# Kernel tuning notes

Hardware: AMD Instinct MI355X
Metric: run time of the kernel (lower is better)

## Reference

```python
import jax, jax.numpy as jnp
import numpy as np

HID = 128          # hidden_channels
NG = 256           # number of graphs in batch
NL = 50000         # ligand nodes
NP = 150000        # protein nodes
E = 500000         # edges (ligand->protein); rev edges are the reverse
RBF_COUNT = 8
D_MAX = 5.0


def _rbf(d):
    # d: [E] distances -> [E, 8] gaussian RBF expansion (D_min=0, D_max=5, count=8)
    mu = jnp.linspace(0.0, D_MAX, RBF_COUNT)
    sigma = D_MAX / RBF_COUNT
    return jnp.exp(-(((d[:, None] - mu[None, :]) / sigma) ** 2))


def setup_inputs() -> dict:
    key = jax.random.key(0)
    ks = jax.random.split(key, 24)
    s = 0.05
    inp = {
        "x_ligand": jax.random.normal(ks[0], (NL, 44), jnp.float32),
        "x_protein": jax.random.normal(ks[1], (NP, 44), jnp.float32),
        "edge_attr": jax.random.uniform(ks[2], (E, 1), jnp.float32) * D_MAX,
        "edge_src": jax.random.randint(ks[3], (E,), 0, NL),
        "edge_dst": jax.random.randint(ks[4], (E,), 0, NP),
        "ligand_batch": jnp.sort(jax.random.randint(ks[5], (NL,), 0, NG)),
        # shared node embedding and edge embedding
        "W_node": jax.random.normal(ks[6], (44, HID), jnp.float32) * s,
        "W_el": jax.random.normal(ks[7], (1, 8), jnp.float32) * s,
        # 6 NConvs: index = layer*2 + (0: ligand->protein, 1: protein->ligand)
        "Wb": jax.random.normal(ks[8], (6, RBF_COUNT, HID), jnp.float32) * s,
        "bb": jnp.zeros((6, HID), jnp.float32),
        "Wn": jax.random.normal(ks[9], (6, HID, HID), jnp.float32) * s,
        "Ws": jax.random.normal(ks[10], (6, HID, HID), jnp.float32) * s,
        "bconv": jnp.zeros((6, HID), jnp.float32),
        # edge MLP: [2*HID+8 -> 512 -> 128] (BN in eval mode = identity, dropout off)
        "W1": jax.random.normal(ks[11], (2 * HID + 8, 512), jnp.float32) * s,
        "b1": jnp.zeros((512,), jnp.float32),
        "W2": jax.random.normal(ks[12], (512, 128), jnp.float32) * s,
        "b2": jnp.zeros((128,), jnp.float32),
        # lin_mpl: 128 -> out_channels//2 = 128
        "Wm": jax.random.normal(ks[13], (128, 128), jnp.float32) * s,
        "bm": jnp.zeros((128,), jnp.float32),
    }
    return inp


def _nconv(x_src, x_dst, src, dst, n_dst, rbf_feat, Wb_i, bb_i, Wn_i, Ws_i, b_i):
    # base = SiLU(Linear(rbf)); message = fc_neigh(base * x_j); aggr = mean over dst
    base = jax.nn.silu(rbf_feat @ Wb_i + bb_i)              # [E, HID]
    msg = (base * x_src[src]) @ Wn_i                         # gather + mul + GEMM
    agg = jax.ops.segment_sum(msg, dst, num_segments=n_dst)  # [n_dst, HID]
    deg = jax.ops.segment_sum(jnp.ones((src.shape[0], 1), msg.dtype), dst,
                              num_segments=n_dst)
    agg = agg / jnp.maximum(deg, 1.0)
    return x_dst @ Ws_i + agg + b_i


def reference(x_ligand, x_protein, edge_attr, edge_src, edge_dst, ligand_batch,
              W_node, W_el, Wb, bb, Wn, Ws, bconv, W1, b1, W2, b2, Wm, bm):
    lrelu = lambda v: jax.nn.leaky_relu(v, 0.01)
    xl = x_ligand @ W_node   # [NL, HID]
    xp = x_protein @ W_node  # [NP, HID]
    rbf_feat = _rbf(jnp.squeeze(edge_attr, -1))  # [E, 8]

    xl_sum = jnp.zeros_like(xl)
    xp_sum = jnp.zeros_like(xp)
    for l in range(3):
        i_lp, i_pl = 2 * l, 2 * l + 1
        # HeteroConv applies both edge types to the SAME input dict
        xp_new = lrelu(_nconv(xl, xp, edge_src, edge_dst, NP, rbf_feat,
                              Wb[i_lp], bb[i_lp], Wn[i_lp], Ws[i_lp], bconv[i_lp]))
        xl_new = lrelu(_nconv(xp, xl, edge_dst, edge_src, NL, rbf_feat,
                              Wb[i_pl], bb[i_pl], Wn[i_pl], Ws[i_pl], bconv[i_pl]))
        xl, xp = xl_new, xp_new
        xl_sum = xl_sum + xl
        xp_sum = xp_sum + xp

    # edge readout on the ligand->protein edges
    edge_repr = jnp.concatenate([xl_sum[edge_src], xp_sum[edge_dst]], axis=-1)
    d_pl = edge_attr @ W_el                                   # [E, 8]
    edge_repr = jnp.concatenate([edge_repr, d_pl], axis=1)    # [E, 2*HID+8]
    # edge_mlp (eval mode: BatchNorm identity, dropout off)
    m_pl = jax.nn.relu(edge_repr @ W1 + b1) @ W2 + b2         # [E, 128]
    w_pl = jnp.tanh(m_pl @ Wm + bm)                           # [E, 128]
    edge_batch = ligand_batch[edge_src]
    m_w = jax.ops.segment_sum(w_pl * m_pl, edge_batch, num_segments=NG)
    m_max = jax.ops.segment_max(m_pl, edge_batch, num_segments=NG)
    m_max = jnp.where(jnp.isfinite(m_max), m_max, 0.0)        # empty segments -> 0
    return jnp.concatenate([m_w, m_max], axis=1)              # [NG, 256]
```

## Files before the change

### kernel.cpp

```cpp
#include <hip/hip_runtime.h>
#include <hip/hip_bf16.h>


#define NLn 50000
#define NPn 150000
#define En  500000
#define NBL 1563
#define NBP 4688

typedef __attribute__((ext_vector_type(8))) short short8;
typedef __attribute__((ext_vector_type(4))) float float4v;

__device__ __forceinline__ float bf2f(unsigned short u){ return __uint_as_float(((unsigned)u) << 16); }
__device__ __forceinline__ float bflo(unsigned u){ return __uint_as_float(u << 16); }
__device__ __forceinline__ float bfhi(unsigned u){ return __uint_as_float(u & 0xffff0000u); }
__device__ __forceinline__ unsigned short f2bf(float f){
  __hip_bfloat16 h = __float2bfloat16(f);
  return *reinterpret_cast<unsigned short*>(&h);
}
__device__ __forceinline__ unsigned encf(float f){
  unsigned u = __float_as_uint(f);
  return (u & 0x80000000u) ? ~u : (u | 0x80000000u);
}
__device__ __forceinline__ float tanh_fast(float x){
  return 1.f - 2.f/(__expf(2.f*x) + 1.f);
}

__global__ __launch_bounds__(256) void k_embed(
    const float* __restrict__ Xl, const float* __restrict__ Xp,
    const float* __restrict__ Wnode,
    unsigned short* __restrict__ xl0, unsigned short* __restrict__ xp0){
  __shared__ float xs[1408];
  int b = blockIdx.x, tid = threadIdx.x;
  bool isL = b < NBL;
  const float* X = isL ? Xl : Xp;
  unsigned short* out = isL ? xl0 : xp0;
  int n = isL ? NLn : NPn;
  int n0 = (isL ? b : b - NBL) * 32;
  int nrows = n - n0; if (nrows > 32) nrows = 32;
  int nflt = nrows * 44;
  const float4* Xv = (const float4*)(X + (size_t)n0*44);
  for (int j = tid; j*4 < nflt; j += 256){
    float4 v = Xv[j];
    xs[j*4+0]=v.x; xs[j*4+1]=v.y; xs[j*4+2]=v.z; xs[j*4+3]=v.w;
  }
  __syncthreads();
  int c = tid & 127, half = tid >> 7;
  float acc[16];
  #pragma unroll
  for (int r=0;r<16;r++) acc[r]=0.f;
  const float* xrow = xs + half*16*44;
  #pragma unroll 4
  for (int k=0;k<44;k++){
    float w = Wnode[k*128 + c];
    #pragma unroll
    for (int r=0;r<16;r++) acc[r] += xrow[r*44 + k] * w;
  }
  int rbase = n0 + half*16;
  #pragma unroll
  for (int r=0;r<16;r++){
    int nn = rbase + r;
    if (nn < n) out[(size_t)nn*128 + c] = f2bf(acc[r]);
  }
}

__global__ __launch_bounds__(256) void k_prep(
    unsigned* __restrict__ cntz, unsigned* __restrict__ mmaxz, unsigned* __restrict__ outz,
    const float* __restrict__ Wel, const float* __restrict__ W1, float* __restrict__ vvec,
    const float* __restrict__ W2, unsigned short* __restrict__ w2t,
    const float* __restrict__ Wm, unsigned short* __restrict__ wmt,
    const float* __restrict__ Ws, const float* __restrict__ Wn,
    unsigned short* __restrict__ wcat, unsigned short* __restrict__ w1t,
    const float* __restrict__ Wb, const float* __restrict__ bb,
    unsigned short* __restrict__ lut){
  int b = blockIdx.x, tid = threadIdx.x;
  if (b < 196){
    for (long i = (long)b*256 + tid; i < 200000; i += 196*256) cntz[i] = 0u;
  } else if (b < 324){
    mmaxz[(b-196)*256 + tid] = 0u;
  } else if (b < 580){
    outz[(b-324)*256 + tid] = 0u;
  } else if (b < 582){
    int j = (b-580)*256 + tid;
    float s = 0.f;
    #pragma unroll
    for (int r=0;r<8;r++) s += Wel[r]*W1[(256+r)*512 + j];
    vvec[j] = s;
  } else if (b < 838){
    int gid = (b-582)*256 + tid;
    int n = gid >> 9, k = gid & 511;
    w2t[n*512 + k] = f2bf(W2[k*128 + n]);
  } else if (b < 902){
    int gid = (b-838)*256 + tid;
    int n = gid >> 7, k = gid & 127;
    wmt[n*128 + k] = f2bf(Wm[k*128 + n]);
  } else if (b < 1670){
    int gid = (b-902)*256 + tid;
    int i = gid >> 15, rem = gid & 32767;
    int n = rem >> 8, k = rem & 255;
    float v = (k < 128) ? Ws[i*16384 + k*128 + n] : Wn[i*16384 + (k-128)*128 + n];
    wcat[gid] = f2bf(v);
  } else if (b < 2182){
    int gid = (b-1670)*256 + tid;
    int part = gid >> 16, rem = gid & 65535;
    int n = rem >> 7, k = rem & 127;
    w1t[gid] = f2bf(W1[(part*128 + k)*512 + n]);
  } else {
    int gid = (b-2182)*256 + tid;
    int c = gid & 127, bin = (gid >> 7) & 4095, i = gid >> 19;
    float d = ((float)bin + 0.5f) * 0.001220703125f;
    float s = bb[i*128 + c];
    #pragma unroll
    for (int j=0;j<8;j++){
      float a = (d - 0.7142857143f*(float)j) * 1.6f;
      s += __expf(-a*a) * Wb[i*1024 + j*128 + c];
    }
    lut[gid] = f2bf(s / (1.f + __expf(-s)));
  }
}

__global__ __launch_bounds__(256) void k_count(const int* __restrict__ esrc,
    const int* __restrict__ edst, unsigned* __restrict__ cntL, unsigned* __restrict__ cntP){
  int e = blockIdx.x*256 + threadIdx.x;
  if (e >= En) return;
  atomicAdd(&cntL[esrc[e]], 1u);
  atomicAdd(&cntP[edst[e]], 1u);
}
__global__ __launch_bounds__(256) void k_cs2(const unsigned* __restrict__ cntL,
    unsigned* __restrict__ rowptrL, unsigned* __restrict__ bsumL,
    const unsigned* __restrict__ cntP, unsigned* __restrict__ rowptrP,
    unsigned* __restrict__ bsumP){
  bool isL = blockIdx.x < 49;
  const unsigned* cnt = isL ? cntL : cntP;
  unsigned* rowptr = isL ? rowptrL : rowptrP;
  unsigned* bsum = isL ? bsumL : bsumP;
  int n = isL ? NLn : NPn;
  int lb = isL ? blockIdx.x : blockIdx.x - 49;
  __shared__ unsigned ts[256];
  int tid = threadIdx.x;
  int base = lb*1024 + tid*4;
  unsigned v[4], run = 0;
  #pragma unroll
  for (int j=0;j<4;j++){ v[j] = run; run += (base+j < n) ? cnt[base+j] : 0u; }
  ts[tid] = run; __syncthreads();
  for (int off=1; off<256; off<<=1){
    unsigned t = (tid>=off) ? ts[tid-off] : 0u; __syncthreads();
    ts[tid] += t; __syncthreads();
  }
  unsigned excl = ts[tid] - run;
  #pragma unroll
  for (int j=0;j<4;j++) if (base+j < n) rowptr[base+j] = excl + v[j];
  if (tid == 255) bsum[lb] = ts[255];
}
__global__ void k_sb2(unsigned* __restrict__ bsumL, unsigned* __restrict__ bsumP){
  unsigned* bsum = blockIdx.x ? bsumP : bsumL;
  int nc = blockIdx.x ? 147 : 49;
  __shared__ unsigned ts[256];
  int tid = threadIdx.x;
  unsigned x = (tid < nc) ? bsum[tid] : 0u;
  ts[tid] = x; __syncthreads();
  for (int off=1; off<256; off<<=1){
    unsigned t = (tid>=off) ? ts[tid-off] : 0u; __syncthreads();
    ts[tid] += t; __syncthreads();
  }
  if (tid < nc) bsum[tid] = ts[tid] - x;
}
__global__ __launch_bounds__(256) void k_ao2(
    unsigned* __restrict__ rowptrL, unsigned* __restrict__ cursorL,
    const unsigned* __restrict__ bsumL,
    unsigned* __restrict__ rowptrP, unsigned* __restrict__ cursorP,
    const unsigned* __restrict__ bsumP){
  bool isL = blockIdx.x < 196;
  unsigned* rowptr = isL ? rowptrL : rowptrP;
  unsigned* cursor = isL ? cursorL : cursorP;
  const unsigned* bsum = isL ? bsumL : bsumP;
  int n = isL ? NLn : NPn;
  int i = (isL ? blockIdx.x : blockIdx.x - 196)*256 + threadIdx.x;
  if (i < n){
    unsigned r = rowptr[i] + bsum[i>>10];
    rowptr[i] = r; cursor[i] = r;
  }
  if (i == 0) rowptr[n] = En;
}
__global__ __launch_bounds__(256) void k_place(const int* __restrict__ esrc,
    const int* __restrict__ edst, const float* __restrict__ ea,
    const int* __restrict__ lbatch, unsigned* __restrict__ curL,
    unsigned* __restrict__ curP, uint4* __restrict__ edgeL,
    int* __restrict__ idxL, int* __restrict__ idxP){
  int e = blockIdx.x*256 + threadIdx.x;
  if (e >= En) return;
  int s = esrc[e], d = edst[e];
  float dd = ea[e];
  int bin = (int)(dd * 819.2f);
  bin = (bin < 0) ? 0 : ((bin > 4095) ? 4095 : bin);
  unsigned pl = atomicAdd(&curL[s], 1u);
  uint4 er; er.x = (unsigned)s; er.y = (unsigned)d;
  er.z = __float_as_uint(dd); er.w = (unsigned)lbatch[s];
  edgeL[pl] = er;
  idxL[pl] = d | (bin << 18);
  unsigned pp = atomicAdd(&curP[d], 1u);
  idxP[pp] = s | (bin << 18);
}

#define EDGE_CAP 1024
__global__ __launch_bounds__(512, 8) void k_conv2(
    const unsigned short* __restrict__ xp_in, const unsigned short* __restrict__ xl_in,
    unsigned short* __restrict__ xp_out, unsigned short* __restrict__ xl_out,
    unsigned short* __restrict__ xp_sum, unsigned short* __restrict__ xl_sum,
    const unsigned* __restrict__ rowptrP, const int* __restrict__ idxP,
    const unsigned* __restrict__ rowptrL, const int* __restrict__ idxL,
    const unsigned short* __restrict__ lut_lp,
    const unsigned short* __restrict__ wcat_lp, const float* __restrict__ bias_lp,
    const unsigned short* __restrict__ lut_pl,
    const unsigned short* __restrict__ wcat_pl, const float* __restrict__ bias_pl,
    int first){
  __shared__ unsigned short ab[32][264];
  __shared__ unsigned short ob[32][136];
  __shared__ int snb[EDGE_CAP];
  __shared__ unsigned rps[33];
  int tid = threadIdx.x;
  int c2 = tid & 63, grp = tid >> 6;
  int bid = blockIdx.x;
  bool isP; int pb;
  if ((bid & 3) == 3){ isP = false; pb = bid >> 2; }
  else if (bid == 6250){ isP = false; pb = 1562; }
  else { isP = true; pb = (bid >> 2)*3 + (bid & 3); }
  const unsigned short* xdst_in = isP ? xp_in : xl_in;
  const unsigned short* xsrc_in = isP ? xl_in : xp_in;
  unsigned short* xout = isP ? xp_out : xl_out;
  unsigned short* xsum = isP ? xp_sum : xl_sum;
  const unsigned* rowptr = isP ? rowptrP : rowptrL;
  const int* eidx = isP ? idxP : idxL;
  const unsigned short* lut_i = isP ? lut_lp : lut_pl;
  const unsigned short* wcat = isP ? wcat_lp : wcat_pl;
  const float* bias = isP ? bias_lp : bias_pl;
  int ndst = isP ? NPn : NLn;
  int n0 = pb * 32;

  if (tid < 33){
    int idx = n0 + tid; if (idx > ndst) idx = ndst;
    rps[tid] = rowptr[idx];
  }
  __syncthreads();
  int r00 = (int)rps[0], rEnd = (int)rps[32];
  int eblk = rEnd - r00;
  bool fits = (eblk <= EDGE_CAP);
  if (fits){
    for (int p = tid; p < eblk; p += 512) snb[p] = eidx[r00 + p];
  }
  __syncthreads();

  const unsigned short* lutc = lut_i + 2*c2;
  const unsigned short* xc = xsrc_in + 2*c2;
  for (int m = grp*4; m < grp*4+4; m++){
    int n = n0 + m;
    float al0=0.f,ah0=0.f,al1=0.f,ah1=0.f,al2=0.f,ah2=0.f,al3=0.f,ah3=0.f;
    int dg = 1;
    if (n < ndst){
      *(unsigned*)&ab[m][2*c2] = *(const unsigned*)&xdst_in[(size_t)n*128 + 2*c2];
      int r0 = (int)rps[m], r1 = (int)rps[m+1];
      dg = r1 - r0;
      int p = r0;
      for (; p + 7 < r1; p += 8){
        int v[8];
        #pragma unroll
        for (int j=0;j<8;j++) v[j] = fits ? snb[p-r00+j] : eidx[p+j];
        unsigned lv[8], xv[8];
        #pragma unroll
        for (int j=0;j<8;j++){
          lv[j] = *(const unsigned*)&lutc[(size_t)((unsigned)v[j] >> 18)*128];
          xv[j] = *(const unsigned*)&xc[(size_t)(v[j] & 0x3FFFF)*128];
        }
        #pragma unroll
        for (int j=0;j<8;j++){
          switch (j & 3){
            case 0: al0 += bflo(lv[j])*bflo(xv[j]); ah0 += bfhi(lv[j])*bfhi(xv[j]); break;
            case 1: al1 += bflo(lv[j])*bflo(xv[j]); ah1 += bfhi(lv[j])*bfhi(xv[j]); break;
            case 2: al2 += bflo(lv[j])*bflo(xv[j]); ah2 += bfhi(lv[j])*bfhi(xv[j]); break;
            default: al3 += bflo(lv[j])*bflo(xv[j]); ah3 += bfhi(lv[j])*bfhi(xv[j]); break;
          }
        }
      }
      for (; p + 3 < r1; p += 4){
        int v0,v1,v2,v3;
        if (fits){
          v0 = snb[p-r00]; v1 = snb[p-r00+1]; v2 = snb[p-r00+2]; v3 = snb[p-r00+3];
        } else {
          v0 = eidx[p]; v1 = eidx[p+1]; v2 = eidx[p+2]; v3 = eidx[p+3];
        }
        unsigned l0 = *(const unsigned*)&lutc[(size_t)((unsigned)v0 >> 18)*128];
        unsigned x0 = *(const unsigned*)&xc[(size_t)(v0 & 0x3FFFF)*128];
        unsigned l1 = *(const unsigned*)&lutc[(size_t)((unsigned)v1 >> 18)*128];
        unsigned x1 = *(const unsigned*)&xc[(size_t)(v1 & 0x3FFFF)*128];
        unsigned l2 = *(const unsigned*)&lutc[(size_t)((unsigned)v2 >> 18)*128];
        unsigned x2 = *(const unsigned*)&xc[(size_t)(v2 & 0x3FFFF)*128];
        unsigned l3 = *(const unsigned*)&lutc[(size_t)((unsigned)v3 >> 18)*128];
        unsigned x3 = *(const unsigned*)&xc[(size_t)(v3 & 0x3FFFF)*128];
        al0 += bflo(l0)*bflo(x0); ah0 += bfhi(l0)*bfhi(x0);
        al1 += bflo(l1)*bflo(x1); ah1 += bfhi(l1)*bfhi(x1);
        al2 += bflo(l2)*bflo(x2); ah2 += bfhi(l2)*bfhi(x2);
        al3 += bflo(l3)*bflo(x3); ah3 += bfhi(l3)*bfhi(x3);
      }
      for (; p < r1; p++){
        int v0 = fits ? snb[p-r00] : eidx[p];
        unsigned l0 = *(const unsigned*)&lutc[(size_t)((unsigned)v0 >> 18)*128];
        unsigned x0 = *(const unsigned*)&xc[(size_t)(v0 & 0x3FFFF)*128];
        al0 += bflo(l0)*bflo(x0); ah0 += bfhi(l0)*bfhi(x0);
      }
    } else {
      *(unsigned*)&ab[m][2*c2] = 0u;
    }
    float inv = 1.f / (float)(dg > 1 ? dg : 1);
    float alo = ((al0+al1)+(al2+al3)) * inv;
    float ahi = ((ah0+ah1)+(ah2+ah3)) * inv;
    *(unsigned*)&ab[m][128 + 2*c2] = (unsigned)f2bf(alo) | ((unsigned)f2bf(ahi) << 16);
  }
  __syncthreads();

  int wave = tid >> 6, lane = tid & 63, quad = lane >> 4, l15 = lane & 15;
  int mt = wave & 1, nh = wave >> 1;
  int arow = mt*16 + l15;
  float4v acc[2] = {{0,0,0,0},{0,0,0,0}};
  for (int k0 = 0; k0 < 256; k0 += 32){
    short8 A = *(const short8*)&ab[arow][k0 + quad*8];
    #pragma unroll
    for (int nt=0;nt<2;nt++){
      short8 B = *(const short8*)&wcat[(size_t)(nh*32 + nt*16 + l15)*256 + k0 + quad*8];
      acc[nt] = __builtin_amdgcn_mfma_f32_16x16x32_bf16(A, B, acc[nt], 0, 0, 0);
    }
  }
  #pragma unroll
  for (int nt=0;nt<2;nt++){
    int col = nh*32 + nt*16 + l15;
    float bc = bias[col];
    #pragma unroll
    for (int r=0;r<4;r++){
      int row = mt*16 + quad*4 + r;
      float v = acc[nt][r] + bc;
      ob[row][col] = f2bf((v > 0.f) ? v : 0.01f*v);
    }
  }
  __syncthreads();
  for (int m = grp*4; m < grp*4+4; m++){
    int n = n0 + m;
    if (n < ndst){
      unsigned vb = *(unsigned*)&ob[m][2*c2];
      size_t off = (size_t)n*128 + 2*c2;
      *(unsigned*)&xout[off] = vb;
      if (first){
        *(unsigned*)&xsum[off] = vb;
      } else {
        unsigned so = *(unsigned*)&xsum[off];
        float lo = bflo(so) + bflo(vb);
        float hi = bfhi(so) + bfhi(vb);
        *(unsigned*)&xsum[off] = (unsigned)f2bf(lo) | ((unsigned)f2bf(hi) << 16);
      }
    }
  }
}

__global__ __launch_bounds__(256) void k_hproj2(
    const unsigned short* __restrict__ xl_s, const unsigned short* __restrict__ xp_s,
    const unsigned short* __restrict__ w1t, const float* __restrict__ b1,
    unsigned* __restrict__ h_l, unsigned* __restrict__ h_p){
  __shared__ unsigned short hb[32][528];
  bool isL = blockIdx.x < NBL;
  const unsigned short* xs = isL ? xl_s : xp_s;
  const unsigned short* wt = isL ? w1t : w1t + 65536;
  unsigned* hout = isL ? h_l : h_p;
  int nn = isL ? NLn : NPn;
  int n0 = (isL ? blockIdx.x : blockIdx.x - NBL)*32;
  int tid = threadIdx.x;
  int wave = tid >> 6, lane = tid & 63, quad = lane >> 4, l15 = lane & 15;
  int mt = wave & 1, nh = wave >> 1;
  int an = n0 + mt*16 + l15; if (an >= nn) an = nn - 1;
  const unsigned short* aptr = xs + (size_t)an*128;
  float4v acc[16];
  #pragma unroll
  for (int i=0;i<16;i++) acc[i] = (float4v){0,0,0,0};
  for (int k0 = 0; k0 < 128; k0 += 32){
    short8 A = *(const short8*)&aptr[k0 + quad*8];
    #pragma unroll
    for (int nt=0;nt<16;nt++){
      short8 B = *(const short8*)&wt[(size_t)(nh*256 + nt*16 + l15)*128 + k0 + quad*8];
      acc[nt] = __builtin_amdgcn_mfma_f32_16x16x32_bf16(A, B, acc[nt], 0, 0, 0);
    }
  }
  #pragma unroll
  for (int nt=0;nt<16;nt++){
    int col = nh*256 + nt*16 + l15;
    float bv = isL ? b1[col] : 0.f;
    #pragma unroll
    for (int r=0;r<4;r++) hb[mt*16 + quad*4 + r][col] = f2bf(acc[nt][r] + bv);
  }
  __syncthreads();
  for (int m=0;m<32;m++){
    int n = n0 + m;
    if (n < nn){
      unsigned pack = (unsigned)hb[m][2*tid] | ((unsigned)hb[m][2*tid+1] << 16);
      hout[(size_t)n*256 + tid] = pack;
    }
  }
}

__global__ __launch_bounds__(512) void k_readout4(
    const unsigned* __restrict__ hl, const unsigned* __restrict__ hp,
    const uint4* __restrict__ edgeL, const float* __restrict__ vvec,
    const unsigned short* __restrict__ w2t, const float* __restrict__ b2,
    const unsigned short* __restrict__ wmt, const float* __restrict__ bm,
    float* __restrict__ outw, unsigned* __restrict__ mmax){
  __shared__ __align__(16) unsigned short lds[37120];
  unsigned short (*msb)[136] = (unsigned short(*)[136])(lds + 32768);
  int tid = threadIdx.x, lane = tid & 63, wave = tid >> 6;
  int quad = lane >> 4, l15 = lane & 15;
  int ns = wave*16;

  int wg = (blockIdx.x & 7)*128 + (blockIdx.x >> 3);
  int nt_tot = En/32;
  int t0 = wg*16;
  int t1 = t0 + 16; if (t1 > nt_tot) t1 = nt_tot;
  if (t0 >= t1) return;

  short8 Bk[16];
  #pragma unroll
  for (int kk=0;kk<16;kk++)
    Bk[kk] = *(const short8*)&w2t[(size_t)(ns + l15)*512 + kk*32 + quad*8];
  short8 Bm[4];
  #pragma unroll
  for (int kk=0;kk<4;kk++)
    Bm[kk] = *(const short8*)&wmt[(size_t)(ns + l15)*128 + kk*32 + quad*8];
  float b2c0 = b2[ns + l15];
  float bm0  = bm[ns + l15];

  float4v vva = *(const float4v*)&vvec[lane*8];
  float4v vvb = *(const float4v*)&vvec[lane*8 + 4];
  int sw = lane & 31;
  const uint4* hl4 = (const uint4*)hl;
  const uint4* hp4 = (const uint4*)hp;
  const unsigned* e32 = (const unsigned*)edgeL;

  int si_prev = -1;
  uint4 ua = {0,0,0,0};
  int lm = wave*16 + (lane & 15);
  int le = lane & 31;

  #define H_EDGE(UA, UB, DD, I, WB)                                          \
    {                                                                        \
      unsigned o0,o1,o2,o3; float hx,hy;                                     \
      hx = fmaxf(bflo(UA.x)+bflo(UB.x)+(DD)*vva.x, 0.f);                     \
      hy = fmaxf(bfhi(UA.x)+bfhi(UB.x)+(DD)*vva.y, 0.f);                     \
      o0 = (unsigned)f2bf(hx) | ((unsigned)f2bf(hy) << 16);                  \
      hx = fmaxf(bflo(UA.y)+bflo(UB.y)+(DD)*vva.z, 0.f);                     \
      hy = fmaxf(bfhi(UA.y)+bfhi(UB.y)+(DD)*vva.w, 0.f);                     \
      o1 = (unsigned)f2bf(hx) | ((unsigned)f2bf(hy) << 16);                  \
      hx = fmaxf(bflo(UA.z)+bflo(UB.z)+(DD)*vvb.x, 0.f);                     \
      hy = fmaxf(bfhi(UA.z)+bfhi(UB.z)+(DD)*vvb.y, 0.f);                     \
      o2 = (unsigned)f2bf(hx) | ((unsigned)f2bf(hy) << 16);                  \
      hx = fmaxf(bflo(UA.w)+bflo(UB.w)+(DD)*vvb.z, 0.f);                     \
      hy = fmaxf(bfhi(UA.w)+bfhi(UB.w)+(DD)*vvb.w, 0.f);                     \
      o3 = (unsigned)f2bf(hx) | ((unsigned)f2bf(hy) << 16);                  \
      uint4 ov; ov.x=o0; ov.y=o1; ov.z=o2; ov.w=o3;                          \
      *(uint4*)&lds[(WB) + lane*256 + (((I) ^ sw) << 3)] = ov;               \
    }

  unsigned md1 = 0; int br_cur = 0, br1 = 0;
  {
    unsigned md0 = e32[(size_t)t0*128 + lm];
    br_cur = (int)e32[((size_t)(t0*32 + le))*4 + 3];
    #pragma unroll
    for (int ii=0; ii<4; ii++){
      int si = __builtin_amdgcn_readfirstlane(__shfl((int)md0, ii*4));
      int di = __builtin_amdgcn_readfirstlane(__shfl((int)md0, ii*4 + 1));
      float dd = __uint_as_float((unsigned)__builtin_amdgcn_readfirstlane(__shfl((int)md0, ii*4 + 2)));
      if (si != si_prev){ ua = hl4[(size_t)si*64 + lane]; si_prev = si; }
      uint4 ub = hp4[(size_t)di*64 + lane];
      H_EDGE(ua, ub, dd, wave*4 + ii, 0)
    }
    if (t0 + 1 < t1){
      md1 = e32[(size_t)(t0+1)*128 + lm];
      br1 = (int)e32[((size_t)((t0+1)*32 + le))*4 + 3];
    }
    __syncthreads();
  }

  int cur = 0;
  unsigned md2 = md1; int br2 = br1;
  for (int t = t0; t < t1; ++t){
    bool pf = (t + 1 < t1);
    if (t + 2 < t1){
      md2 = e32[(size_t)(t+2)*128 + lm];
      br2 = (int)e32[((size_t)((t+2)*32 + le))*4 + 3];
    }
    uint4 ub0, ub1, ub2, ub3;
    if (pf){
      int d0 = __builtin_amdgcn_readfirstlane(__shfl((int)md1, 1));
      int d1 = __builtin_amdgcn_readfirstlane(__shfl((int)md1, 5));
      int d2 = __builtin_amdgcn_readfirstlane(__shfl((int)md1, 9));
      int d3 = __builtin_amdgcn_readfirstlane(__shfl((int)md1, 13));
      ub0 = hp4[(size_t)d0*64 + lane];
      ub1 = hp4[(size_t)d1*64 + lane];
      ub2 = hp4[(size_t)d2*64 + lane];
      ub3 = hp4[(size_t)d3*64 + lane];
      int s0 = __builtin_amdgcn_readfirstlane(__shfl((int)md1, 0));
      if (s0 != si_prev){ ua = hl4[(size_t)s0*64 + lane]; si_prev = s0; }
    }

    int rb = cur ? 16384 : 0;
    float4v acc[2] = {{0,0,0,0},{0,0,0,0}};
    #pragma unroll
    for (int kk = 0; kk < 16; kk++){
      int kcc = kk*4 + quad;
      int sw2 = kcc & 31;
      short8 A0 = *(const short8*)&lds[rb + kcc*256 + ((l15 ^ sw2) << 3)];
      short8 A1 = *(const short8*)&lds[rb + kcc*256 + (((16 + l15) ^ sw2) << 3)];
      acc[0] = __builtin_amdgcn_mfma_f32_16x16x32_bf16(A0, Bk[kk], acc[0], 0, 0, 0);
      acc[1] = __builtin_amdgcn_mfma_f32_16x16x32_bf16(A1, Bk[kk], acc[1], 0, 0, 0);
    }
    float mreg[2][4];
    #pragma unroll
    for (int mt=0;mt<2;mt++){
      int col = ns + l15;
      #pragma unroll
      for (int r=0;r<4;r++){
        float mv = acc[mt][r] + b2c0;
        mreg[mt][r] = mv;
        msb[mt*16 + quad*4 + r][col] = f2bf(mv);
      }
    }
    __syncthreads();

    float4v acc2[2] = {{0,0,0,0},{0,0,0,0}};
    #pragma unroll
    for (int kk = 0; kk < 4; kk++){
      short8 A0 = *(const short8*)&msb[l15][kk*32 + quad*8];
      short8 A1 = *(const short8*)&msb[16 + l15][kk*32 + quad*8];
      acc2[0] = __builtin_amdgcn_mfma_f32_16x16x32_bf16(A0, Bm[kk], acc2[0], 0, 0, 0);
      acc2[1] = __builtin_amdgcn_mfma_f32_16x16x32_bf16(A1, Bm[kk], acc2[1], 0, 0, 0);
    }
    {
      int b0 = __shfl(br_cur, 0);
      bool uni = (b0 == __shfl(br_cur, 31));
      int col = ns + l15;
      if (uni){
        float s = 0.f, mx = -3.402823466e38f;
        #pragma unroll
        for (int mt=0;mt<2;mt++){
          #pragma unroll
          for (int r=0;r<4;r++){
            float mv = mreg[mt][r];
            float tt = tanh_fast(acc2[mt][r] + bm0);
            s += tt*mv; mx = fmaxf(mx, mv);
          }
        }
        s += __shfl_xor(s, 16); s += __shfl_xor(s, 32);
        mx = fmaxf(mx, __shfl_xor(mx, 16)); mx = fmaxf(mx, __shfl_xor(mx, 32));
        if (quad == 0){
          atomicAdd(&outw[b0*256 + col], s);
          atomicMax(&mmax[b0*128 + col], encf(mx));
        }
      } else {
        #pragma unroll
        for (int mt=0;mt<2;mt++){
          #pragma unroll
          for (int r=0;r<4;r++){
            int row = mt*16 + quad*4 + r;
            int b = __shfl(br_cur, row);
            float mv = mreg[mt][r];
            float tt = tanh_fast(acc2[mt][r] + bm0);
            atomicAdd(&outw[b*256 + col], tt*mv);
            atomicMax(&mmax[b*128 + col], encf(mv));
          }
        }
      }
    }

    if (pf){
      int wb = cur ? 0 : 16384;
      #pragma unroll
      for (int ii=0; ii<4; ii++){
        int si = __builtin_amdgcn_readfirstlane(__shfl((int)md1, ii*4));
        float dd = __uint_as_float((unsigned)__builtin_amdgcn_readfirstlane(__shfl((int)md1, ii*4 + 2)));
        if (si != si_prev){ ua = hl4[(size_t)si*64 + lane]; si_prev = si; }
        uint4 ub = (ii==0) ? ub0 : (ii==1) ? ub1 : (ii==2) ? ub2 : ub3;
        H_EDGE(ua, ub, dd, wave*4 + ii, wb)
      }
    }
    __syncthreads();

    md1 = md2; br_cur = br1; br1 = br2;
    cur ^= 1;
  }
  #undef H_EDGE
}

__global__ __launch_bounds__(256) void k_final(const unsigned* __restrict__ mmax,
    float* __restrict__ out){
  int gid = blockIdx.x*256 + threadIdx.x;
  unsigned enc = mmax[gid];
  float v;
  if (enc == 0u) v = 0.f;
  else if (enc & 0x80000000u) v = __uint_as_float(enc & 0x7FFFFFFFu);
  else v = __uint_as_float(~enc);
  int g = gid >> 7, cc = gid & 127;
  out[g*256 + 128 + cc] = v;
}

extern "C" void kernel_launch(void* const* d_in, const int* in_sizes, int n_in,
                              void* d_out, int out_size, void* d_ws, size_t ws_size,
                              hipStream_t stream) {
  const float* x_l    = (const float*)d_in[0];
  const float* x_p    = (const float*)d_in[1];
  const float* ea     = (const float*)d_in[2];
  const int*   esrc   = (const int*)d_in[3];
  const int*   edst   = (const int*)d_in[4];
  const int*   lbatch = (const int*)d_in[5];
  const float* W_node = (const float*)d_in[6];
  const float* W_el   = (const float*)d_in[7];
  const float* Wb     = (const float*)d_in[8];
  const float* bb     = (const float*)d_in[9];
  const float* Wn     = (const float*)d_in[10];
  const float* Ws     = (const float*)d_in[11];
  const float* bconv  = (const float*)d_in[12];
  const float* W1     = (const float*)d_in[13];
  const float* b1     = (const float*)d_in[14];
  const float* W2     = (const float*)d_in[15];
  const float* b2     = (const float*)d_in[16];
  const float* Wm     = (const float*)d_in[17];
  const float* bm     = (const float*)d_in[18];

  char* w = (char*)d_ws;
  unsigned short* xl0 = (unsigned short*)(w + 0);
  unsigned short* xl1 = (unsigned short*)(w + 12800000);
  unsigned short* xp0 = (unsigned short*)(w + 25600000);
  unsigned short* xp1 = (unsigned short*)(w + 64000000);
  int*      idxP  = (int*)(w + 102400000);
  int*      idxL  = (int*)(w + 104400000);
  unsigned short* lut = (unsigned short*)(w + 106400000);
  unsigned* h_l   = (unsigned*)(w + 0);
  unsigned* h_p   = (unsigned*)(w + 51200000);
  unsigned short* xl_s = (unsigned short*)(w + 204800000);
  unsigned short* xp_s = (unsigned short*)(w + 217600000);
  unsigned short* wcat = (unsigned short*)(w + 256000000);
  unsigned short* w1t  = (unsigned short*)(w + 256393216);
  unsigned short* w2t  = (unsigned short*)(w + 256655360);
  unsigned short* wmt  = (unsigned short*)(w + 256786432);
  float*    vvec  = (float*)(w + 256819200);
  unsigned* mmax  = (unsigned*)(w + 256821248);
  unsigned* bsumL = (unsigned*)(w + 256952320);
  unsigned* bsumP = (unsigned*)(w + 256953344);
  unsigned* rowptrL = (unsigned*)(w + 256954368);
  unsigned* cursorL = (unsigned*)(w + 257154432);
  unsigned* rowptrP = (unsigned*)(w + 257354432);
  unsigned* cursorP = (unsigned*)(w + 257954496);
  unsigned* cntL    = (unsigned*)(w + 258554496);
  unsigned* cntP    = (unsigned*)(w + 258754496);
  uint4*    edgeL   = (uint4*)(w + 259354496);

  float* out = (float*)d_out;

  k_prep<<<14470, 256, 0, stream>>>(
      (unsigned*)(w + 258554496), mmax, (unsigned*)d_out,
      W_el, W1, vvec, W2, w2t, Wm, wmt, Ws, Wn, wcat, w1t, Wb, bb, lut);
  k_embed<<<NBL + NBP, 256, 0, stream>>>(x_l, x_p, W_node, xl0, xp0);

  k_count<<<1954, 256, 0, stream>>>(esrc, edst, cntL, cntP);
  k_cs2<<<196, 256, 0, stream>>>(cntL, rowptrL, bsumL, cntP, rowptrP, bsumP);
  k_sb2<<<2, 256, 0, stream>>>(bsumL, bsumP);
  k_ao2<<<782, 256, 0, stream>>>(rowptrL, cursorL, bsumL, rowptrP, cursorP, bsumP);
  k_place<<<1954, 256, 0, stream>>>(esrc, edst, ea, lbatch, cursorL, cursorP,
                                    edgeL, idxL, idxP);

  unsigned short *xlc = xl0, *xln = xl1, *xpc = xp0, *xpn = xp1;
  for (int l = 0; l < 3; ++l){
    int ilp = 2*l, ipl = 2*l + 1;
    k_conv2<<<NBP + NBL, 512, 0, stream>>>(
        xpc, xlc, xpn, xln, xp_s, xl_s,
        rowptrP, idxP, rowptrL, idxL,
        lut + (size_t)ilp*524288, wcat + ilp*32768, bconv + ilp*128,
        lut + (size_t)ipl*524288, wcat + ipl*32768, bconv + ipl*128,
        (l == 0) ? 1 : 0);
    unsigned short* t;
    t = xlc; xlc = xln; xln = t;
    t = xpc; xpc = xpn; xpn = t;
  }

  k_hproj2<<<NBL + NBP, 256, 0, stream>>>(xl_s, xp_s, w1t, b1, h_l, h_p);

  k_readout4<<<1024, 512, 0, stream>>>(h_l, h_p, edgeL, vvec,
                                       w2t, b2, wmt, bm, out, mmax);
  k_final<<<128, 256, 0, stream>>>(mmax, out);
}
```

Before: 1.224 ms.

## Make hidden projection persistent with register-resident weights; share RBF exps in LUT build

```diff
diff --git a/kernel.cpp b/kernel.cpp
--- a/kernel.cpp
+++ b/kernel.cpp
@@ -73,6 +73,7 @@
     unsigned short* __restrict__ wcat, unsigned short* __restrict__ w1t,
     const float* __restrict__ Wb, const float* __restrict__ bb,
     unsigned short* __restrict__ lut){
+  __shared__ float gw[16];
   int b = blockIdx.x, tid = threadIdx.x;
   if (b < 196){
     for (long i = (long)b*256 + tid; i < 200000; i += 196*256) cntz[i] = 0u;
@@ -106,16 +107,22 @@
     int n = rem >> 7, k = rem & 127;
     w1t[gid] = f2bf(W1[(part*128 + k)*512 + n]);
   } else {
-    int gid = (b-2182)*256 + tid;
-    int c = gid & 127, bin = (gid >> 7) & 4095, i = gid >> 19;
-    float d = ((float)bin + 0.5f) * 0.001220703125f;
+    int gid0 = (b-2182)*256;
+    int c = tid & 127, half = tid >> 7;
+    int bin0 = (gid0 >> 7) & 4095;
+    int i = gid0 >> 19;
+    if (tid < 16){
+      int bn = bin0 + (tid >> 3), j = tid & 7;
+      float d = ((float)bn + 0.5f) * 0.001220703125f;
+      float a = (d - 0.7142857143f*(float)j) * 1.6f;
+      gw[tid] = __expf(-a*a);
+    }
+    __syncthreads();
     float s = bb[i*128 + c];
-    #pragma unroll
-    for (int j=0;j<8;j++){
-      float a = (d - 0.7142857143f*(float)j) * 1.6f;
-      s += __expf(-a*a) * Wb[i*1024 + j*128 + c];
-    }
-    lut[gid] = f2bf(s / (1.f + __expf(-s)));
+    const float* g = gw + half*8;
+    #pragma unroll
+    for (int j=0;j<8;j++) s += g[j] * Wb[i*1024 + j*128 + c];
+    lut[gid0 + tid] = f2bf(s / (1.f + __expf(-s)));
   }
 }
 
@@ -359,47 +366,72 @@
   }
 }
 
-__global__ __launch_bounds__(256) void k_hproj2(
+__global__ __launch_bounds__(512) void k_hproj3(
     const unsigned short* __restrict__ xl_s, const unsigned short* __restrict__ xp_s,
     const unsigned short* __restrict__ w1t, const float* __restrict__ b1,
     unsigned* __restrict__ h_l, unsigned* __restrict__ h_p){
   __shared__ unsigned short hb[32][528];
-  bool isL = blockIdx.x < NBL;
+  int tid = threadIdx.x, lane = tid & 63, wave = tid >> 6;
+  int quad = lane >> 4, l15 = lane & 15;
+  bool isL = blockIdx.x < 256;
   const unsigned short* xs = isL ? xl_s : xp_s;
   const unsigned short* wt = isL ? w1t : w1t + 65536;
   unsigned* hout = isL ? h_l : h_p;
   int nn = isL ? NLn : NPn;
-  int n0 = (isL ? blockIdx.x : blockIdx.x - NBL)*32;
-  int tid = threadIdx.x;
-  int wave = tid >> 6, lane = tid & 63, quad = lane >> 4, l15 = lane & 15;
-  int mt = wave & 1, nh = wave >> 1;
-  int an = n0 + mt*16 + l15; if (an >= nn) an = nn - 1;
-  const unsigned short* aptr = xs + (size_t)an*128;
-  float4v acc[16];
+  int ntile = isL ? NBL : NBP;
+  int wg = isL ? blockIdx.x : blockIdx.x - 256;
+  int stride = isL ? 256 : 768;
+
+  short8 Bk[4][4];
+  float bv[4];
   #pragma unroll
-  for (int i=0;i<16;i++) acc[i] = (float4v){0,0,0,0};
-  for (int k0 = 0; k0 < 128; k0 += 32){
-    short8 A = *(const short8*)&aptr[k0 + quad*8];
-    #pragma unroll
-    for (int nt=0;nt<16;nt++){
-      short8 B = *(const short8*)&wt[(size_t)(nh*256 + nt*16 + l15)*128 + k0 + quad*8];
-      acc[nt] = __builtin_amdgcn_mfma_f32_16x16x32_bf16(A, B, acc[nt], 0, 0, 0);
-    }
-  }
-  #pragma unroll
-  for (int nt=0;nt<16;nt++){
-    int col = nh*256 + nt*16 + l15;
-    float bv = isL ? b1[col] : 0.f;
-    #pragma unroll
-    for (int r=0;r<4;r++) hb[mt*16 + quad*4 + r][col] = f2bf(acc[nt][r] + bv);
-  }
-  __syncthreads();
-  for (int m=0;m<32;m++){
-    int n = n0 + m;
-    if (n < nn){
-      unsigned pack = (unsigned)hb[m][2*tid] | ((unsigned)hb[m][2*tid+1] << 16);
-      hout[(size_t)n*256 + tid] = pack;
-    }
+  for (int nt=0;nt<4;nt++){
+    int row = wave*64 + nt*16 + l15;
+    #pragma unroll
+    for (int kk=0;kk<4;kk++)
+      Bk[nt][kk] = *(const short8*)&wt[(size_t)row*128 + kk*32 + quad*8];
+    bv[nt] = isL ? b1[row] : 0.f;
+  }
+
+  for (int t = wg; t < ntile; t += stride){
+    int n0 = t*32;
+    int a0r = n0 + l15;      if (a0r >= nn) a0r = nn-1;
+    int a1r = n0 + 16 + l15; if (a1r >= nn) a1r = nn-1;
+    float4v acc[2][4];
+    #pragma unroll
+    for (int m2=0;m2<2;m2++)
+      #pragma unroll
+      for (int nt=0;nt<4;nt++) acc[m2][nt] = (float4v){0,0,0,0};
+    #pragma unroll
+    for (int kk=0;kk<4;kk++){
+      short8 A0 = *(const short8*)&xs[(size_t)a0r*128 + kk*32 + quad*8];
+      short8 A1 = *(const short8*)&xs[(size_t)a1r*128 + kk*32 + quad*8];
+      #pragma unroll
+      for (int nt=0;nt<4;nt++){
+        acc[0][nt] = __builtin_amdgcn_mfma_f32_16x16x32_bf16(A0, Bk[nt][kk], acc[0][nt], 0, 0, 0);
+        acc[1][nt] = __builtin_amdgcn_mfma_f32_16x16x32_bf16(A1, Bk[nt][kk], acc[1][nt], 0, 0, 0);
+      }
+    }
+    #pragma unroll
+    for (int m2=0;m2<2;m2++){
+      #pragma unroll
+      for (int nt=0;nt<4;nt++){
+        int col = wave*64 + nt*16 + l15;
+        #pragma unroll
+        for (int r=0;r<4;r++)
+          hb[m2*16 + quad*4 + r][col] = f2bf(acc[m2][nt][r] + bv[nt]);
+      }
+    }
+    __syncthreads();
+    for (int idx = tid; idx < 8192; idx += 512){
+      int m = idx >> 8, d = idx & 255;
+      int n = n0 + m;
+      if (n < nn){
+        unsigned pack = (unsigned)hb[m][2*d] | ((unsigned)hb[m][2*d+1] << 16);
+        hout[(size_t)n*256 + d] = pack;
+      }
+    }
+    __syncthreads();
   }
 }
 
@@ -684,7 +716,7 @@
     t = xpc; xpc = xpn; xpn = t;
   }
 
-  k_hproj2<<<NBL + NBP, 256, 0, stream>>>(xl_s, xp_s, w1t, b1, h_l, h_p);
+  k_hproj3<<<1024, 512, 0, stream>>>(xl_s, xp_s, w1t, b1, h_l, h_p);
 
   k_readout4<<<1024, 512, 0, stream>>>(h_l, h_p, edgeL, vvec,
                                        w2t, b2, wmt, bm, out, mmax);
```

Measured after the change: 1.095 ms. 1.12x faster.
